# Performance work log

Hardware: AMD Instinct MI355X
Metric: run time of the kernel (lower is better)

Reference implementation:

```python
import jax, jax.numpy as jnp
import numpy as np

H = 16      # query heads
G = 4       # kv heads
D = 64      # head dim
ROPE_BASE = 10000.0

def _rotate_half(t):
    t1, t2 = jnp.split(t, 2, axis=-1)
    return jnp.concatenate([-t2, t1], axis=-1)

def _rope_emb(n):
    inv_freq = 1.0 / (ROPE_BASE ** (jnp.arange(0, D, 2, dtype=jnp.float32) / D))
    freqs = jnp.outer(jnp.arange(n, dtype=jnp.float32), inv_freq)  # [n, D/2]
    return jnp.concatenate([freqs, freqs], axis=-1)               # [n, D]

def setup_inputs() -> dict:
    key = jax.random.key(0)
    k1, k2, k3, k4 = jax.random.split(key, 4)
    B, N, C = 2, 2048, 1024
    x = jax.random.normal(k1, (B, N, C), dtype=jnp.float32)
    w_q = jax.random.normal(k2, (C, C), dtype=jnp.float32) * 0.02
    w_kv = jax.random.normal(k3, (C, 2 * G * D), dtype=jnp.float32) * 0.02
    w_out = jax.random.normal(k4, (C, C), dtype=jnp.float32) * 0.02
    return {"x": x, "w_q": w_q, "w_kv": w_kv, "w_out": w_out}

def reference(x, w_q, w_kv, w_out):
    B, N, C = x.shape
    scale = D ** -0.5
    q = (x @ w_q).reshape(B, N, H, D).transpose(0, 2, 1, 3)        # [B,H,N,D]
    kv = x @ w_kv
    k, v = jnp.split(kv, 2, axis=-1)
    k = k.reshape(B, N, G, D).transpose(0, 2, 1, 3)                # [B,G,N,D]
    v = v.reshape(B, N, G, D).transpose(0, 2, 1, 3)
    emb = _rope_emb(N)                                             # [N,D]
    cos, sin = jnp.cos(emb), jnp.sin(emb)
    q = q * cos + _rotate_half(q) * sin
    k = k * cos + _rotate_half(k) * sin
    # NOTE: faithful to source einsum -- kv-head axis g is SUMMED (absent from output)
    scores = jnp.einsum('bhid,bgjd->bhij', q, k) * scale           # [B,H,N,N]
    probs = jax.nn.softmax(scores, axis=-1)
    out = jnp.einsum('bhij,bgjd->bhid', probs, v)                  # [B,H,N,D]
    out = out.transpose(0, 2, 1, 3).reshape(B, N, H * D)
    return out @ w_out
```

## Files before the change

kernel.cpp:

```cpp
#include <hip/hip_runtime.h>
#include <hip/hip_bf16.h>
#include <math.h>

#define B_ 2
#define N_ 2048
#define C_ 1024
#define H_ 16
#define G_ 4
#define D_ 64
#define QKV_N 1152

#define QSCALE 0.18033688011112042f

using short8  = __attribute__((ext_vector_type(8))) short;
using short4v = __attribute__((ext_vector_type(4))) short;
using float4v = __attribute__((ext_vector_type(4))) float;

#if __has_builtin(__builtin_amdgcn_mfma_f32_16x16x16_bf16)
#define MFMA16K16(A, B, C) __builtin_amdgcn_mfma_f32_16x16x16_bf16(A, B, C, 0, 0, 0)
#else
#define MFMA16K16(A, B, C) __builtin_amdgcn_mfma_f32_16x16x16bf16_1k(A, B, C, 0, 0, 0)
#endif

__device__ __forceinline__ ushort f2bf(float f) {
    union { float f; unsigned u; } v; v.f = f;
    unsigned r = (v.u + 0x7FFF + ((v.u >> 16) & 1)) >> 16;
    return (ushort)r;
}
__device__ __forceinline__ float bf2f(ushort u) {
    union { unsigned u; float f; } t; t.u = ((unsigned)u) << 16; return t.f;
}
__device__ __forceinline__ unsigned pack_bf16(float a, float b) {
#if __has_builtin(__builtin_amdgcn_cvt_pk_bf16_f32)
    auto t = __builtin_amdgcn_cvt_pk_bf16_f32(a, b);
    unsigned r; __builtin_memcpy(&r, &t, 4); return r;
#else
    return (unsigned)f2bf(a) | ((unsigned)f2bf(b) << 16);
#endif
}
__device__ __forceinline__ float fexp2(float x) {
#if __has_builtin(__builtin_amdgcn_exp2f)
    return __builtin_amdgcn_exp2f(x);
#else
    return exp2f(x);
#endif
}

__device__ void tconv_body(const float* __restrict__ src, ushort* __restrict__ dst,
                           int K, int N, int bx, int by, float (*T)[65]) {
    const int n0 = bx * 64, k0 = by * 64;
    const int tid = threadIdx.x;
    #pragma unroll
    for (int s = 0; s < 16; ++s) {
        int idx = tid + s * 256; int r = idx >> 6, cc = idx & 63;
        T[r][cc] = src[(size_t)(k0 + r) * N + n0 + cc];
    }
    __syncthreads();
    #pragma unroll
    for (int s = 0; s < 16; ++s) {
        int idx = tid + s * 256; int r = idx >> 6, cc = idx & 63;
        dst[(size_t)(n0 + r) * K + k0 + cc] = f2bf(T[cc][r]);
    }
}

__global__ void prep(const float* __restrict__ x, const float* __restrict__ w_q,
                     const float* __restrict__ w_kv, const float* __restrict__ w_out,
                     ushort* __restrict__ xb, ushort* __restrict__ wqkvT,
                     ushort* __restrict__ woutT) {
    __shared__ float T[64][65];
    const int blk = blockIdx.x, tid = threadIdx.x;
    if (blk < 4096) {
        int i = blk * 1024 + tid * 4;
        float4 v = *(const float4*)(x + i);
        ushort4 o;
        o.x = f2bf(v.x); o.y = f2bf(v.y); o.z = f2bf(v.z); o.w = f2bf(v.w);
        *(ushort4*)(xb + i) = o;
    } else if (blk < 4352) {
        int idx = blk - 4096;
        tconv_body(w_q, wqkvT, C_, C_, idx & 15, idx >> 4, T);
    } else if (blk < 4608) {
        int idx = blk - 4352;
        tconv_body(w_out, woutT, C_, C_, idx & 15, idx >> 4, T);
    } else {
        const int k0 = (blk - 4608) * 64;
        #pragma unroll
        for (int it = 0; it < 4; ++it) {
            int p = tid + it * 256;
            int kk = p >> 4, d4 = (p & 15) * 4;
            float ks[4] = {0, 0, 0, 0}, vs[4] = {0, 0, 0, 0};
            #pragma unroll
            for (int g = 0; g < G_; ++g) {
                float4 a = *(const float4*)(w_kv + (size_t)(k0 + kk) * 512 + g * 64 + d4);
                float4 b = *(const float4*)(w_kv + (size_t)(k0 + kk) * 512 + 256 + g * 64 + d4);
                ks[0] += a.x; ks[1] += a.y; ks[2] += a.z; ks[3] += a.w;
                vs[0] += b.x; vs[1] += b.y; vs[2] += b.z; vs[3] += b.w;
            }
            #pragma unroll
            for (int e = 0; e < 4; ++e) {
                wqkvT[(size_t)(1024 + d4 + e) * C_ + k0 + kk] = f2bf(ks[e]);
                wqkvT[(size_t)(1088 + d4 + e) * C_ + k0 + kk] = f2bf(vs[e]);
            }
        }
    }
}

template <int MODE>
__global__ __launch_bounds__(256) void gemm128p(const ushort* __restrict__ A,
                                                const ushort* __restrict__ Bt,
                                                void* __restrict__ Cv,
                                                ushort* __restrict__ Kt,
                                                ushort* __restrict__ VtT,
                                                int M, int N, int K) {
    __shared__ __align__(16) ushort As[2][128 * 64];
    __shared__ __align__(16) ushort Bs[2][64 * 64];

    const int tid = threadIdx.x, wave = tid >> 6, lane = tid & 63;
    const int g = lane >> 4, c = lane & 15;
    const int m0 = blockIdx.y * 128, n0 = blockIdx.x * 64;

    const int lr = tid >> 3;
    const int lq = tid & 7;
    const int gsw = (lq ^ (lr & 7)) * 8;
    const ushort* pa = A  + (size_t)(m0 + lr) * K + gsw;
    const ushort* pb = Bt + (size_t)(n0 + lr) * K + gsw;

    auto stage = [&](int buf, int k0) {
        #pragma unroll
        for (int i = 0; i < 4; ++i)
            __builtin_amdgcn_global_load_lds(
                (const __attribute__((address_space(1))) void*)(pa + (size_t)i * 32 * K + k0),
                (__attribute__((address_space(3))) void*)&As[buf][(i * 32 + wave * 8) * 64], 16, 0, 0);
        #pragma unroll
        for (int i = 0; i < 2; ++i)
            __builtin_amdgcn_global_load_lds(
                (const __attribute__((address_space(1))) void*)(pb + (size_t)i * 32 * K + k0),
                (__attribute__((address_space(3))) void*)&Bs[buf][(i * 32 + wave * 8) * 64], 16, 0, 0);
    };

    float4v acc[2][4];
    #pragma unroll
    for (int m = 0; m < 2; ++m)
        #pragma unroll
        for (int n = 0; n < 4; ++n) acc[m][n] = {0, 0, 0, 0};

    stage(0, 0);
    __syncthreads();

    const int NT = K >> 6;
    int cur = 0;
    for (int t = 0; t < NT; ++t) {
        if (t + 1 < NT) stage(cur ^ 1, (t + 1) << 6);

        #pragma unroll
        for (int kk = 0; kk < 2; ++kk) {
            const int c7 = c & 7;
            short8 af[2], bf[4];
            #pragma unroll
            for (int m = 0; m < 2; ++m)
                af[m] = *(const short8*)&As[cur][(wave * 32 + m * 16 + c) * 64 + ((kk * 4 + g) ^ c7) * 8];
            #pragma unroll
            for (int n = 0; n < 4; ++n)
                bf[n] = *(const short8*)&Bs[cur][(n * 16 + c) * 64 + ((kk * 4 + g) ^ c7) * 8];
            #pragma unroll
            for (int m = 0; m < 2; ++m)
                #pragma unroll
                for (int n = 0; n < 4; ++n)
                    acc[m][n] = __builtin_amdgcn_mfma_f32_16x16x32_bf16(af[m], bf[n], acc[m][n], 0, 0, 0);
        }
        __syncthreads();
        cur ^= 1;
    }

    if (MODE == 1) {
        if (blockIdx.x < 16) {
            const float invf_e = __powf(10000.0f, -(float)c * (1.0f / 32.0f));
            const float invf_o = __powf(10000.0f, -(float)(c + 16) * (1.0f / 32.0f));
            #pragma unroll
            for (int m = 0; m < 2; ++m)
                #pragma unroll
                for (int r = 0; r < 4; ++r) {
                    const int rowi = m0 + wave * 32 + m * 16 + 4 * g + r;
                    const float nf = (float)(rowi & (N_ - 1));
                    float sn0, cs0, sn1, cs1;
                    __sincosf(nf * invf_e, &sn0, &cs0);
                    __sincosf(nf * invf_o, &sn1, &cs1);
                    #pragma unroll
                    for (int nn = 0; nn < 4; ++nn) {
                        const float v = acc[m][nn][r], p = acc[m][nn ^ 2][r];
                        const float rh = (nn < 2) ? -p : p;
                        const float sn = (nn & 1) ? sn1 : sn0;
                        const float cs = (nn & 1) ? cs1 : cs0;
                        ((ushort*)Cv)[(size_t)rowi * N + n0 + nn * 16 + c] =
                            f2bf((v * cs + rh * sn) * QSCALE);
                    }
                }
            return;
        }
        if (blockIdx.x == 16) {
            const float invf_e = __powf(10000.0f, -(float)c * (1.0f / 32.0f));
            const float invf_o = __powf(10000.0f, -(float)(c + 16) * (1.0f / 32.0f));
            #pragma unroll
            for (int m = 0; m < 2; ++m)
                #pragma unroll
                for (int r = 0; r < 4; ++r) {
                    const int rowi = m0 + wave * 32 + m * 16 + 4 * g + r;
                    const float nf = (float)(rowi & (N_ - 1));
                    float sn0, cs0, sn1, cs1;
                    __sincosf(nf * invf_e, &sn0, &cs0);
                    __sincosf(nf * invf_o, &sn1, &cs1);
                    #pragma unroll
                    for (int nn = 0; nn < 4; ++nn) {
                        const float v = acc[m][nn][r], p = acc[m][nn ^ 2][r];
                        const float rh = (nn < 2) ? -p : p;
                        const float sn = (nn & 1) ? sn1 : sn0;
                        const float cs = (nn & 1) ? cs1 : cs0;
                        Kt[(size_t)rowi * 64 + nn * 16 + c] = f2bf(v * cs + rh * sn);
                    }
                }
        } else {
            #pragma unroll
            for (int m = 0; m < 2; ++m)
                #pragma unroll
                for (int nn = 0; nn < 4; ++nn)
                    #pragma unroll
                    for (int r = 0; r < 4; ++r) {
                        const int rowi = m0 + wave * 32 + m * 16 + 4 * g + r;
                        const int n = rowi & (N_ - 1), bb = rowi >> 11;
                        VtT[((size_t)bb * 64 + nn * 16 + c) * N_ + n] = f2bf(acc[m][nn][r]);
                    }
        }
        return;
    }

    #pragma unroll
    for (int m = 0; m < 2; ++m)
        #pragma unroll
        for (int n = 0; n < 4; ++n)
            #pragma unroll
            for (int r = 0; r < 4; ++r) {
                int rowi = m0 + wave * 32 + m * 16 + 4 * g + r;
                int coli = n0 + n * 16 + c;
                ((float*)Cv)[(size_t)rowi * N + coli] = acc[m][n][r];
            }
}

__global__ __launch_bounds__(512) void attn16(
        const ushort* __restrict__ qkvb, const ushort* __restrict__ Kt,
        const ushort* __restrict__ VtT,
        ushort* __restrict__ oP0, ushort* __restrict__ oP1,
        float* __restrict__ lP0, float* __restrict__ lP1) {
    const int s  = blockIdx.x & 1;
    const int qt = (blockIdx.x >> 1) & 7;
    const int h  = (blockIdx.x >> 4) & 15;
    const int b  = blockIdx.x >> 8;
    const int tid = threadIdx.x, wave = tid >> 6, lane = tid & 63;
    const int g = lane >> 4, c = lane & 15;

    __shared__ __align__(16) ushort Ksh[64 * 64];
    __shared__ __align__(16) ushort Vsh[64 * 64];

    ushort* oPs = s ? oP1 : oP0;
    float*  lPs = s ? lP1 : lP0;

    const int i0 = qt * 256 + wave * 32;

    short8 qf[2][2];
    #pragma unroll
    for (int a = 0; a < 2; ++a) {
        const int row = i0 + a * 16 + c;
        const ushort* qrow = qkvb + (size_t)(b * N_ + row) * QKV_N + h * 64;
        qf[a][0] = *(const short8*)(qrow + 8 * g);
        qf[a][1] = *(const short8*)(qrow + 32 + 8 * g);
    }

    float4v o[2][4];
    #pragma unroll
    for (int a = 0; a < 2; ++a)
        #pragma unroll
        for (int f = 0; f < 4; ++f) o[a][f] = {0, 0, 0, 0};
    float ll[2] = {0.f, 0.f};

    const ushort* Kb = Kt  + (size_t)b * N_ * 64;
    const ushort* Vb = VtT + (size_t)b * 64 * N_;
    const int lr8 = lane >> 3, lq8 = lane & 7;
    const int wpos = (lq8 ^ lr8) * 8;
    const int j0 = s * (N_ / 2);
    const int NT = (N_ / 2) / 64;

    short8 kr0 = *(const short8*)(Kb + (size_t)(j0 + wave * 8 + lr8) * 64 + lq8 * 8);
    short8 vr0 = *(const short8*)(Vb + (size_t)(wave * 8 + lr8) * N_ + j0 + lq8 * 8);

    for (int t = 0; t < NT; ++t) {
        __syncthreads();
        *(short8*)&Ksh[(wave * 8 + lr8) * 64 + wpos] = kr0;
        *(short8*)&Vsh[(wave * 8 + lr8) * 64 + wpos] = vr0;
        __syncthreads();
        if (t + 1 < NT) {
            const int jn = j0 + (t + 1) * 64;
            kr0 = *(const short8*)(Kb + (size_t)(jn + wave * 8 + lr8) * 64 + lq8 * 8);
            vr0 = *(const short8*)(Vb + (size_t)(wave * 8 + lr8) * N_ + jn + lq8 * 8);
        }

        #pragma unroll
        for (int jt4 = 0; jt4 < 4; ++jt4) {
            const int R = jt4 * 16 + c;
            short8 kf0 = *(const short8*)&Ksh[R * 64 + ((g ^ (c & 7)) * 8)];
            short8 kf1 = *(const short8*)&Ksh[R * 64 + (((g ^ 4) ^ (c & 7)) * 8)];
            short4v vf[4];
            #pragma unroll
            for (int f = 0; f < 4; ++f)
                vf[f] = *(const short4v*)&Vsh[(16 * f + c) * 64 +
                          (((jt4 * 2 + (g >> 1)) ^ (c & 7)) * 8) + (g & 1) * 4];

            #pragma unroll
            for (int a = 0; a < 2; ++a) {
                float4v st = {0, 0, 0, 0};
                st = __builtin_amdgcn_mfma_f32_16x16x32_bf16(kf0, qf[a][0], st, 0, 0, 0);
                st = __builtin_amdgcn_mfma_f32_16x16x32_bf16(kf1, qf[a][1], st, 0, 0, 0);
                float p0 = fexp2(st[0]), p1 = fexp2(st[1]);
                float p2 = fexp2(st[2]), p3 = fexp2(st[3]);
                ll[a] += (p0 + p1) + (p2 + p3);
                union { unsigned u[2]; short4v v; } pk;
                pk.u[0] = pack_bf16(p0, p1);
                pk.u[1] = pack_bf16(p2, p3);
                #pragma unroll
                for (int f = 0; f < 4; ++f)
                    o[a][f] = MFMA16K16(vf[f], pk.v, o[a][f]);
            }
        }
    }

    #pragma unroll
    for (int a = 0; a < 2; ++a) {
        float lt = ll[a];
        lt += __shfl_xor(lt, 16, 64);
        lt += __shfl_xor(lt, 32, 64);
        const int row = i0 + a * 16 + c;
        if (g == 0) lPs[(size_t)(b * N_ + row) * 16 + h] = lt;
        #pragma unroll
        for (int f = 0; f < 4; ++f) {
            ushort4 w;
            w.x = f2bf(o[a][f][0]); w.y = f2bf(o[a][f][1]);
            w.z = f2bf(o[a][f][2]); w.w = f2bf(o[a][f][3]);
            *(ushort4*)(oPs + (size_t)(b * N_ + row) * 1024 + h * 64 + 16 * f + 4 * g) = w;
        }
    }
}

__global__ void combine(const ushort* __restrict__ oP0, const ushort* __restrict__ oP1,
                        const float* __restrict__ lP0, const float* __restrict__ lP1,
                        ushort* __restrict__ ao) {
    const int e = (blockIdx.x * 256 + threadIdx.x) * 4;
    const int row = e >> 10, hh = (e >> 6) & 15;
    const float inv = 1.0f / (lP0[row * 16 + hh] + lP1[row * 16 + hh]);
    ushort4 a = *(const ushort4*)(oP0 + e);
    ushort4 b = *(const ushort4*)(oP1 + e);
    ushort4 r;
    r.x = f2bf((bf2f(a.x) + bf2f(b.x)) * inv);
    r.y = f2bf((bf2f(a.y) + bf2f(b.y)) * inv);
    r.z = f2bf((bf2f(a.z) + bf2f(b.z)) * inv);
    r.w = f2bf((bf2f(a.w) + bf2f(b.w)) * inv);
    *(ushort4*)(ao + e) = r;
}

extern "C" void kernel_launch(void* const* d_in, const int* in_sizes, int n_in,
                              void* d_out, int out_size, void* d_ws, size_t ws_size,
                              hipStream_t stream) {
    const float* x     = (const float*)d_in[0];
    const float* w_q   = (const float*)d_in[1];
    const float* w_kv  = (const float*)d_in[2];
    const float* w_out = (const float*)d_in[3];
    float* out = (float*)d_out;

    const int M = B_ * N_;
    ushort* xb    = (ushort*)d_ws;
    ushort* wqkvT = xb    + (size_t)M * C_;
    ushort* woutT = wqkvT + (size_t)QKV_N * C_;
    ushort* qkvb  = woutT + (size_t)C_ * C_;
    ushort* Kt    = qkvb  + (size_t)M * QKV_N;
    ushort* VtT   = Kt    + (size_t)B_ * N_ * D_;
    ushort* oP1   = VtT   + (size_t)B_ * D_ * N_;
    float*  lP0   = (float*)(oP1 + (size_t)M * C_);
    float*  lP1   = lP0 + (size_t)M * H_;
    ushort* oP0   = xb;
    ushort* ao    = xb;

    prep<<<4624, 256, 0, stream>>>(x, w_q, w_kv, w_out, xb, wqkvT, woutT);
    gemm128p<1><<<dim3(QKV_N / 64, M / 128), 256, 0, stream>>>(xb, wqkvT, qkvb, Kt, VtT, M, QKV_N, C_);
    attn16<<<B_ * H_ * (N_ / 256) * 2, 512, 0, stream>>>(qkvb, Kt, VtT, oP0, oP1, lP0, lP1);
    combine<<<(M * C_) / 1024, 256, 0, stream>>>(oP0, oP1, lP0, lP1, ao);
    gemm128p<2><<<dim3(C_ / 64, M / 128), 256, 0, stream>>>(ao, woutT, out, nullptr, nullptr, M, C_, C_);
}
```

Measured before the change: 179.8 us.

## Drop split-KV attention and combine kernel; normalize output in attention epilogue

```diff
diff --git a/kernel.cpp b/kernel.cpp
--- a/kernel.cpp
+++ b/kernel.cpp
@@ -244,23 +244,17 @@
             }
 }
 
-__global__ __launch_bounds__(512) void attn16(
+__global__ __launch_bounds__(512) void attn17(
         const ushort* __restrict__ qkvb, const ushort* __restrict__ Kt,
-        const ushort* __restrict__ VtT,
-        ushort* __restrict__ oP0, ushort* __restrict__ oP1,
-        float* __restrict__ lP0, float* __restrict__ lP1) {
-    const int s  = blockIdx.x & 1;
-    const int qt = (blockIdx.x >> 1) & 7;
-    const int h  = (blockIdx.x >> 4) & 15;
-    const int b  = blockIdx.x >> 8;
+        const ushort* __restrict__ VtT, ushort* __restrict__ ao) {
+    const int qt = blockIdx.x & 7;
+    const int h  = (blockIdx.x >> 3) & 15;
+    const int b  = blockIdx.x >> 7;
     const int tid = threadIdx.x, wave = tid >> 6, lane = tid & 63;
     const int g = lane >> 4, c = lane & 15;
 
     __shared__ __align__(16) ushort Ksh[64 * 64];
     __shared__ __align__(16) ushort Vsh[64 * 64];
-
-    ushort* oPs = s ? oP1 : oP0;
-    float*  lPs = s ? lP1 : lP0;
 
     const int i0 = qt * 256 + wave * 32;
 
@@ -284,11 +278,10 @@
     const ushort* Vb = VtT + (size_t)b * 64 * N_;
     const int lr8 = lane >> 3, lq8 = lane & 7;
     const int wpos = (lq8 ^ lr8) * 8;
-    const int j0 = s * (N_ / 2);
-    const int NT = (N_ / 2) / 64;
-
-    short8 kr0 = *(const short8*)(Kb + (size_t)(j0 + wave * 8 + lr8) * 64 + lq8 * 8);
-    short8 vr0 = *(const short8*)(Vb + (size_t)(wave * 8 + lr8) * N_ + j0 + lq8 * 8);
+    const int NT = N_ / 64;
+
+    short8 kr0 = *(const short8*)(Kb + (size_t)(wave * 8 + lr8) * 64 + lq8 * 8);
+    short8 vr0 = *(const short8*)(Vb + (size_t)(wave * 8 + lr8) * N_ + lq8 * 8);
 
     for (int t = 0; t < NT; ++t) {
         __syncthreads();
@@ -296,7 +289,7 @@
         *(short8*)&Vsh[(wave * 8 + lr8) * 64 + wpos] = vr0;
         __syncthreads();
         if (t + 1 < NT) {
-            const int jn = j0 + (t + 1) * 64;
+            const int jn = (t + 1) * 64;
             kr0 = *(const short8*)(Kb + (size_t)(jn + wave * 8 + lr8) * 64 + lq8 * 8);
             vr0 = *(const short8*)(Vb + (size_t)(wave * 8 + lr8) * N_ + jn + lq8 * 8);
         }
@@ -335,32 +328,16 @@
         float lt = ll[a];
         lt += __shfl_xor(lt, 16, 64);
         lt += __shfl_xor(lt, 32, 64);
+        const float inv = 1.0f / lt;
         const int row = i0 + a * 16 + c;
-        if (g == 0) lPs[(size_t)(b * N_ + row) * 16 + h] = lt;
         #pragma unroll
         for (int f = 0; f < 4; ++f) {
             ushort4 w;
-            w.x = f2bf(o[a][f][0]); w.y = f2bf(o[a][f][1]);
-            w.z = f2bf(o[a][f][2]); w.w = f2bf(o[a][f][3]);
-            *(ushort4*)(oPs + (size_t)(b * N_ + row) * 1024 + h * 64 + 16 * f + 4 * g) = w;
-        }
-    }
-}
-
-__global__ void combine(const ushort* __restrict__ oP0, const ushort* __restrict__ oP1,
-                        const float* __restrict__ lP0, const float* __restrict__ lP1,
-                        ushort* __restrict__ ao) {
-    const int e = (blockIdx.x * 256 + threadIdx.x) * 4;
-    const int row = e >> 10, hh = (e >> 6) & 15;
-    const float inv = 1.0f / (lP0[row * 16 + hh] + lP1[row * 16 + hh]);
-    ushort4 a = *(const ushort4*)(oP0 + e);
-    ushort4 b = *(const ushort4*)(oP1 + e);
-    ushort4 r;
-    r.x = f2bf((bf2f(a.x) + bf2f(b.x)) * inv);
-    r.y = f2bf((bf2f(a.y) + bf2f(b.y)) * inv);
-    r.z = f2bf((bf2f(a.z) + bf2f(b.z)) * inv);
-    r.w = f2bf((bf2f(a.w) + bf2f(b.w)) * inv);
-    *(ushort4*)(ao + e) = r;
+            w.x = f2bf(o[a][f][0] * inv); w.y = f2bf(o[a][f][1] * inv);
+            w.z = f2bf(o[a][f][2] * inv); w.w = f2bf(o[a][f][3] * inv);
+            *(ushort4*)(ao + (size_t)(b * N_ + row) * 1024 + h * 64 + 16 * f + 4 * g) = w;
+        }
+    }
 }
 
 extern "C" void kernel_launch(void* const* d_in, const int* in_sizes, int n_in,
@@ -379,15 +356,10 @@
     ushort* qkvb  = woutT + (size_t)C_ * C_;
     ushort* Kt    = qkvb  + (size_t)M * QKV_N;
     ushort* VtT   = Kt    + (size_t)B_ * N_ * D_;
-    ushort* oP1   = VtT   + (size_t)B_ * D_ * N_;
-    float*  lP0   = (float*)(oP1 + (size_t)M * C_);
-    float*  lP1   = lP0 + (size_t)M * H_;
-    ushort* oP0   = xb;
     ushort* ao    = xb;
 
     prep<<<4624, 256, 0, stream>>>(x, w_q, w_kv, w_out, xb, wqkvT, woutT);
     gemm128p<1><<<dim3(QKV_N / 64, M / 128), 256, 0, stream>>>(xb, wqkvT, qkvb, Kt, VtT, M, QKV_N, C_);
-    attn16<<<B_ * H_ * (N_ / 256) * 2, 512, 0, stream>>>(qkvb, Kt, VtT, oP0, oP1, lP0, lP1);
-    combine<<<(M * C_) / 1024, 256, 0, stream>>>(oP0, oP1, lP0, lP1, ao);
+    attn17<<<B_ * H_ * (N_ / 256), 512, 0, stream>>>(qkvb, Kt, VtT, ao);
     gemm128p<2><<<dim3(C_ / 64, M / 128), 256, 0, stream>>>(ao, woutT, out, nullptr, nullptr, M, C_, C_);
 }
```

New measurement: 172.0 us. -4.3%, faster.
